# Optimization experiments

Measured on AMD Instinct MI355X. Metric: run time of the kernel, lower is better.

## Reference

```python
import jax, jax.numpy as jnp
import numpy as np

D_MODEL = 1024
NUM_HEADS = 16
DEPTH = D_MODEL // NUM_HEADS
MAX_LEN = 5000


def _make_pe(d_model=D_MODEL, max_len=MAX_LEN):
    # Faithful to torch PositionalEncoding: pe shape [max_len, 1, d_model]
    position = np.arange(max_len, dtype=np.float32)[:, None]
    div_term = np.exp(np.arange(0, d_model, 2, dtype=np.float32) * (-np.log(10000.0) / d_model))
    pe = np.zeros((max_len, d_model), dtype=np.float32)
    pe[:, 0::2] = np.sin(position * div_term)
    pe[:, 1::2] = np.cos(position * div_term)
    return jnp.asarray(pe[:, None, :])  # [max_len, 1, d_model]


def setup_inputs() -> dict:
    key = jax.random.key(0)
    ks = jax.random.split(key, 11)
    B, S, D = 4, 2048, D_MODEL
    s = 1.0 / np.sqrt(D)
    inp = {
        "v": jax.random.normal(ks[0], (B, S, D), jnp.float32),
        "k": jax.random.normal(ks[1], (B, S, D), jnp.float32),
        "q": jax.random.normal(ks[2], (B, S, D), jnp.float32),
        "wq_w": jax.random.normal(ks[3], (D, D), jnp.float32) * s,
        "wq_b": jnp.zeros((D,), jnp.float32),
        "wk_w": jax.random.normal(ks[4], (D, D), jnp.float32) * s,
        "wk_b": jnp.zeros((D,), jnp.float32),
        "wv_w": jax.random.normal(ks[5], (D, D), jnp.float32) * s,
        "wv_b": jnp.zeros((D,), jnp.float32),
        "dense_w": jax.random.normal(ks[6], (D, D), jnp.float32) * s,
        "dense_b": jnp.zeros((D,), jnp.float32),
        "pe": _make_pe(),
    }
    return inp


def _split_heads(x, B):
    # [B, S, D] -> [B, H, S, depth]
    return x.reshape(B, -1, NUM_HEADS, DEPTH).transpose(0, 2, 1, 3)


def reference(v, k, q, wq_w, wq_b, wk_w, wk_b, wv_w, wv_b, dense_w, dense_b, pe):
    B = q.shape[0]
    # Faithful bug-reproduction: pe[:batch] has shape [B, 1, D], broadcast over seq.
    pe_b = pe[:B]  # [B, 1, D]
    q = q + pe_b
    k = k + pe_b
    v = v + pe_b
    # Linear layers (torch: x @ W.T + b)
    qh = _split_heads(q @ wq_w.T + wq_b, B)  # [B,H,Sq,d]
    kh = _split_heads(k @ wk_w.T + wk_b, B)  # [B,H,Sk,d]
    vh = _split_heads(v @ wv_w.T + wv_b, B)  # [B,H,Sk,d]
    scale = 1.0 / jnp.sqrt(jnp.float32(DEPTH))
    logits = jnp.einsum("bhqd,bhkd->bhqk", qh, kh) * scale
    attn = jax.nn.softmax(logits, axis=-1)
    out = jnp.einsum("bhqk,bhkd->bhqd", attn, vh)
    out = out.transpose(0, 2, 1, 3).reshape(B, -1, D_MODEL)
    return out @ dense_w.T + dense_b
```

## Files before the change

### kernel.cpp

```cpp
#include <hip/hip_runtime.h>
#include <hip/hip_bf16.h>

typedef short short8 __attribute__((ext_vector_type(8)));
typedef float f32x4 __attribute__((ext_vector_type(4)));
typedef float f32x16 __attribute__((ext_vector_type(16)));
typedef unsigned int uint4v __attribute__((ext_vector_type(4)));

#define MFMA16(a, b, c) __builtin_amdgcn_mfma_f32_16x16x32_bf16(a, b, c, 0, 0, 0)
#define MFMA32(a, b, c) __builtin_amdgcn_mfma_f32_32x32x16_bf16(a, b, c, 0, 0, 0)

typedef __attribute__((address_space(1))) const unsigned int gas_u32;
typedef __attribute__((address_space(3))) unsigned int las_u32;

__device__ inline void gll16(const void* g, void* l) {
    __builtin_amdgcn_global_load_lds((gas_u32*)g, (las_u32*)l, 16, 0, 0);
}

__device__ inline unsigned short f2bf(float f) {
    unsigned u = __builtin_bit_cast(unsigned, f);
    u += 0x7fff + ((u >> 16) & 1);
    return (unsigned short)(u >> 16);
}

__device__ inline unsigned pk_trunc(float a, float b) {
    unsigned ua = __builtin_bit_cast(unsigned, a);
    unsigned ub = __builtin_bit_cast(unsigned, b);
    return (ua >> 16) | (ub & 0xFFFF0000u);
}

__device__ inline float exp2_fast(float x) {
#if __has_builtin(__builtin_amdgcn_exp2f)
    return __builtin_amdgcn_exp2f(x);
#else
    float r; asm("v_exp_f32 %0, %1" : "=v"(r) : "v"(x)); return r;
#endif
}

__device__ inline void pl32_swap(unsigned &a, unsigned &b) {
    asm volatile("v_permlane32_swap_b32 %0, %1" : "+v"(a), "+v"(b));
}

__global__ void pe_cast3(const float* __restrict__ q, const float* __restrict__ k,
                         const float* __restrict__ v, const float* __restrict__ pe,
                         unsigned short* __restrict__ oq, unsigned short* __restrict__ ok,
                         unsigned short* __restrict__ ov) {
    const float* x = (blockIdx.y == 0) ? q : (blockIdx.y == 1) ? k : v;
    unsigned short* o = (blockIdx.y == 0) ? oq : (blockIdx.y == 1) ? ok : ov;
    int i = blockIdx.x * 256 + threadIdx.x;
    long e = (long)i * 4;
    int b = (int)(e >> 21);
    int d = (int)(e & 1023);
    float4 xv = reinterpret_cast<const float4*>(x)[i];
    float4 pv = *reinterpret_cast<const float4*>(pe + b * 1024 + d);
    ushort4 r;
    r.x = f2bf(xv.x + pv.x); r.y = f2bf(xv.y + pv.y);
    r.z = f2bf(xv.z + pv.z); r.w = f2bf(xv.w + pv.w);
    reinterpret_cast<ushort4*>(o)[i] = r;
}

__global__ void wcast4(const float* __restrict__ w0, const float* __restrict__ w1,
                       const float* __restrict__ w2, const float* __restrict__ w3,
                       unsigned short* __restrict__ o0) {
    const float* w = (blockIdx.y == 0) ? w0 : (blockIdx.y == 1) ? w1
                   : (blockIdx.y == 2) ? w2 : w3;
    unsigned short* o = o0 + (size_t)blockIdx.y * 1024 * 1024;
    int i = blockIdx.x * 256 + threadIdx.x;
    float4 xv = reinterpret_cast<const float4*>(w)[i];
    ushort4 r;
    r.x = f2bf(xv.x); r.y = f2bf(xv.y); r.z = f2bf(xv.z); r.w = f2bf(xv.w);
    reinterpret_cast<ushort4*>(o)[i] = r;
}

__global__ __launch_bounds__(256) void gemm_qkv(const unsigned short* __restrict__ X0,
                                                const unsigned short* __restrict__ W0,
                                                const float* __restrict__ bq,
                                                const float* __restrict__ bk,
                                                const float* __restrict__ bv,
                                                unsigned short* __restrict__ oq,
                                                unsigned short* __restrict__ ok,
                                                unsigned short* __restrict__ ov,
                                                float qscale) {
    const int K = 1024;
    int z = blockIdx.z;
    const unsigned short* A = X0 + (size_t)z * 8192 * 1024;
    const unsigned short* W = W0 + (size_t)z * 1024 * 1024;
    const float* bias = (z == 0) ? bq : (z == 1) ? bk : bv;
    unsigned short* out = (z == 0) ? oq : (z == 1) ? ok : ov;
    float scale = (z == 0) ? qscale : 1.0f;

    __shared__ unsigned short lsA[128 * 32];
    __shared__ unsigned short lsB[128 * 32];
    int tid = threadIdx.x;
    int wave = tid >> 6, lane = tid & 63, lg = lane >> 4, l15 = lane & 15;
    int brow = blockIdx.x * 128;
    int bcol = blockIdx.y * 128;
    int wr = wave >> 1, wc = wave & 1;

    f32x4 zero4 = {0.f, 0.f, 0.f, 0.f};
    f32x4 acc[4][4];
#pragma unroll
    for (int m = 0; m < 4; ++m)
#pragma unroll
        for (int n = 0; n < 4; ++n) acc[m][n] = zero4;

    for (int k0 = 0; k0 < K; k0 += 32) {
#pragma unroll
        for (int j = 0; j < 2; ++j) {
            int c = j * 256 + wave * 64 + lane;
            const unsigned short* srcA = A + ((long)(brow + (c >> 2)) * K + k0 + (c & 3) * 8);
            const unsigned short* srcB = W + ((long)(bcol + (c >> 2)) * K + k0 + (c & 3) * 8);
            char* dstA = (char*)lsA + (j * 256 + wave * 64) * 16;
            char* dstB = (char*)lsB + (j * 256 + wave * 64) * 16;
            gll16(srcA, dstA);
            gll16(srcB, dstB);
        }
        __syncthreads();
        short8 af[4], bf_[4];
#pragma unroll
        for (int m = 0; m < 4; ++m) {
            int row = wr * 64 + m * 16 + l15;
            af[m] = *(const short8*)((const char*)lsA + row * 64 + lg * 16);
        }
#pragma unroll
        for (int n = 0; n < 4; ++n) {
            int col = wc * 64 + n * 16 + l15;
            bf_[n] = *(const short8*)((const char*)lsB + col * 64 + lg * 16);
        }
#pragma unroll
        for (int m = 0; m < 4; ++m)
#pragma unroll
            for (int n = 0; n < 4; ++n) acc[m][n] = MFMA16(af[m], bf_[n], acc[m][n]);
        __syncthreads();
    }

#pragma unroll
    for (int m = 0; m < 4; ++m)
#pragma unroll
        for (int n = 0; n < 4; ++n) {
            int col = bcol + wc * 64 + n * 16 + l15;
            float bv_ = bias[col];
#pragma unroll
            for (int r = 0; r < 4; ++r) {
                int row = brow + wr * 64 + m * 16 + lg * 4 + r;
                float v = (acc[m][n][r] + bv_) * scale;
                int b = row >> 11, s = row & 2047;
                if (z < 2) {
                    int h = col >> 6, d = col & 63;
                    out[(((long)(b * 16 + h) * 2048 + s) * 64 + d)] = f2bf(v);
                } else {
                    out[((long)(b * 1024 + col)) * 2048 + s] = f2bf(v);
                }
            }
        }
}

__global__ __launch_bounds__(256) void gemm_dense(const unsigned short* __restrict__ A,
                                                  const unsigned short* __restrict__ W,
                                                  const float* __restrict__ bias,
                                                  float* __restrict__ out) {
    const int K = 1024;
    __shared__ unsigned short lsA[128 * 32];
    __shared__ unsigned short lsB[128 * 32];
    int tid = threadIdx.x;
    int wave = tid >> 6, lane = tid & 63, lg = lane >> 4, l15 = lane & 15;
    int brow = blockIdx.x * 128;
    int bcol = blockIdx.y * 128;
    int wr = wave >> 1, wc = wave & 1;

    f32x4 zero4 = {0.f, 0.f, 0.f, 0.f};
    f32x4 acc[4][4];
#pragma unroll
    for (int m = 0; m < 4; ++m)
#pragma unroll
        for (int n = 0; n < 4; ++n) acc[m][n] = zero4;

    for (int k0 = 0; k0 < K; k0 += 32) {
#pragma unroll
        for (int j = 0; j < 2; ++j) {
            int c = j * 256 + wave * 64 + lane;
            const unsigned short* srcA = A + ((long)(brow + (c >> 2)) * K + k0 + (c & 3) * 8);
            const unsigned short* srcB = W + ((long)(bcol + (c >> 2)) * K + k0 + (c & 3) * 8);
            char* dstA = (char*)lsA + (j * 256 + wave * 64) * 16;
            char* dstB = (char*)lsB + (j * 256 + wave * 64) * 16;
            gll16(srcA, dstA);
            gll16(srcB, dstB);
        }
        __syncthreads();
        short8 af[4], bf_[4];
#pragma unroll
        for (int m = 0; m < 4; ++m) {
            int row = wr * 64 + m * 16 + l15;
            af[m] = *(const short8*)((const char*)lsA + row * 64 + lg * 16);
        }
#pragma unroll
        for (int n = 0; n < 4; ++n) {
            int col = wc * 64 + n * 16 + l15;
            bf_[n] = *(const short8*)((const char*)lsB + col * 64 + lg * 16);
        }
#pragma unroll
        for (int m = 0; m < 4; ++m)
#pragma unroll
            for (int n = 0; n < 4; ++n) acc[m][n] = MFMA16(af[m], bf_[n], acc[m][n]);
        __syncthreads();
    }

#pragma unroll
    for (int m = 0; m < 4; ++m)
#pragma unroll
        for (int n = 0; n < 4; ++n) {
            int col = bcol + wc * 64 + n * 16 + l15;
            float bv = bias[col];
#pragma unroll
            for (int r = 0; r < 4; ++r) {
                int row = brow + wr * 64 + m * 16 + lg * 4 + r;
                out[(long)row * 1024 + col] = acc[m][n][r] + bv;
            }
        }
}

__global__ __launch_bounds__(256, 2) void attn_kernel(const unsigned short* __restrict__ Qh,
                                                      const unsigned short* __restrict__ Kh,
                                                      const unsigned short* __restrict__ Vt,
                                                      unsigned short* __restrict__ Om) {
    const int S = 2048;
    const int NT = S / 64;
    int flat = blockIdx.x;
    int nf_ = (flat & 7) * 64 + (flat >> 3);
    int qt = nf_ & 7;
    int bh = nf_ >> 3;
    int b = bh >> 4, h = bh & 15;

    int tid = threadIdx.x, wave = tid >> 6, lane = tid & 63;
    int l31 = lane & 31, hi = lane >> 5;

    __shared__ __align__(16) unsigned short Kl[3][4096];
    __shared__ __align__(16) unsigned short Vtl[3][4096];

    const unsigned short* Qb = Qh + (long)bh * S * 64;
    const unsigned short* Kb = Kh + (long)bh * S * 64;
    const unsigned short* Vb = Vt + (long)bh * 64 * S;

    int colS = ((((tid & 7) * 16) ^ (((tid >> 3) & 7) << 4)) >> 1);
    const unsigned short* srcK = Kb + (tid >> 3) * 64 + colS;
    const unsigned short* srcV = Vb + (tid >> 3) * 2048 + colS;

    short8 aq[2][4];
    {
        const unsigned short* qrow = Qb + (long)(qt * 256 + wave * 64 + l31) * 64 + hi * 8;
#pragma unroll
        for (int qf = 0; qf < 2; ++qf)
#pragma unroll
            for (int s = 0; s < 4; ++s)
                aq[qf][s] = *(const short8*)(qrow + qf * 32 * 64 + s * 16);
    }

    f32x16 oacc[2][2], lacc[2];
#pragma unroll
    for (int r = 0; r < 16; ++r) {
        oacc[0][0][r] = 0.f; oacc[0][1][r] = 0.f;
        oacc[1][0][r] = 0.f; oacc[1][1][r] = 0.f;
        lacc[0][r] = 0.f; lacc[1][r] = 0.f;
    }

    const short8 ones8 = {0x3F80, 0x3F80, 0x3F80, 0x3F80, 0x3F80, 0x3F80, 0x3F80, 0x3F80};

    int rb0 = l31 * 128;
    int swz = (l31 & 7) << 4;

#define STAGE(kt, bi) do {                                              \
        const unsigned short* sk = srcK + (kt) * 4096;                  \
        gll16(sk,         (char*)Kl[bi] + wave * 1024);                 \
        gll16(sk + 2048,  (char*)Kl[bi] + 4096 + wave * 1024);          \
        const unsigned short* sv = srcV + (kt) * 64;                    \
        gll16(sv,         (char*)Vtl[bi] + wave * 1024);                \
        gll16(sv + 65536, (char*)Vtl[bi] + 4096 + wave * 1024);         \
    } while (0)

    STAGE(0, 0);
    STAGE(1, 1);

    int bi = 0, sb = 2;
    for (int kt = 0; kt < NT; ++kt) {
        if (kt == NT - 1) { asm volatile("s_waitcnt vmcnt(0)" ::: "memory"); }
        else              { asm volatile("s_waitcnt vmcnt(4)" ::: "memory"); }
        __builtin_amdgcn_s_barrier();
        if (kt < NT - 2) STAGE(kt + 2, sb);

        const char* KlC = (const char*)Kl[bi];
        const char* VlC = (const char*)Vtl[bi];

        f32x16 sacc[2][2];
#pragma unroll
        for (int r = 0; r < 16; ++r) {
            sacc[0][0][r] = 0.f; sacc[0][1][r] = 0.f;
            sacc[1][0][r] = 0.f; sacc[1][1][r] = 0.f;
        }
#pragma unroll
        for (int blk = 0; blk < 2; ++blk)
#pragma unroll
            for (int s = 0; s < 4; ++s) {
                short8 kf = *(const short8*)(KlC + blk * 4096 + rb0 + ((32 * s + 16 * hi) ^ swz));
                sacc[0][blk] = MFMA32(kf, aq[0][s], sacc[0][blk]);
                sacc[1][blk] = MFMA32(kf, aq[1][s], sacc[1][blk]);
            }

#pragma unroll
        for (int qf = 0; qf < 2; ++qf)
#pragma unroll
            for (int blk = 0; blk < 2; ++blk)
#pragma unroll
                for (int r = 0; r < 16; ++r) sacc[qf][blk][r] = exp2_fast(sacc[qf][blk][r]);

#pragma unroll
        for (int s = 0; s < 4; ++s) {
            const int blk = s >> 1, base = (s & 1) * 8;
            short8 pa[2];
#pragma unroll
            for (int qf = 0; qf < 2; ++qf) {
                unsigned q0 = pk_trunc(sacc[qf][blk][base + 0], sacc[qf][blk][base + 1]);
                unsigned q1 = pk_trunc(sacc[qf][blk][base + 2], sacc[qf][blk][base + 3]);
                unsigned q2 = pk_trunc(sacc[qf][blk][base + 4], sacc[qf][blk][base + 5]);
                unsigned q3 = pk_trunc(sacc[qf][blk][base + 6], sacc[qf][blk][base + 7]);
                pl32_swap(q0, q2);
                pl32_swap(q1, q3);
                uint4v pw; pw[0] = q0; pw[1] = q1; pw[2] = q2; pw[3] = q3;
                pa[qf] = __builtin_bit_cast(short8, pw);
            }
#pragma unroll
            for (int dblk = 0; dblk < 2; ++dblk) {
                short8 vf = *(const short8*)(VlC + dblk * 4096 + rb0 + ((32 * s + 16 * hi) ^ swz));
                oacc[0][dblk] = MFMA32(pa[0], vf, oacc[0][dblk]);
                oacc[1][dblk] = MFMA32(pa[1], vf, oacc[1][dblk]);
            }
            lacc[0] = MFMA32(pa[0], ones8, lacc[0]);
            lacc[1] = MFMA32(pa[1], ones8, lacc[1]);
        }
        bi = (bi == 2) ? 0 : bi + 1;
        sb = (sb == 2) ? 0 : sb + 1;
    }
#undef STAGE

#pragma unroll
    for (int qf = 0; qf < 2; ++qf) {
        float inv[16];
#pragma unroll
        for (int r = 0; r < 16; ++r) inv[r] = 1.0f / lacc[qf][r];
        int qrow0 = qt * 256 + wave * 64 + qf * 32 + 4 * hi;
#pragma unroll
        for (int dblk = 0; dblk < 2; ++dblk)
#pragma unroll
            for (int r = 0; r < 16; ++r) {
                int qrow = qrow0 + (r & 3) + 8 * (r >> 2);
                int d = h * 64 + dblk * 32 + l31;
                float v = oacc[qf][dblk][r] * inv[r];
                Om[((long)b * 2048 + qrow) * 1024 + d] = f2bf(v);
            }
    }
}

extern "C" void kernel_launch(void* const* d_in, const int* in_sizes, int n_in,
                              void* d_out, int out_size, void* d_ws, size_t ws_size,
                              hipStream_t stream) {
    const float* v_in = (const float*)d_in[0];
    const float* k_in = (const float*)d_in[1];
    const float* q_in = (const float*)d_in[2];
    const float* wq_w = (const float*)d_in[3];
    const float* wq_b = (const float*)d_in[4];
    const float* wk_w = (const float*)d_in[5];
    const float* wk_b = (const float*)d_in[6];
    const float* wv_w = (const float*)d_in[7];
    const float* wv_b = (const float*)d_in[8];
    const float* wd_w = (const float*)d_in[9];
    const float* wd_b = (const float*)d_in[10];
    const float* pe   = (const float*)d_in[11];

    const long SZ = 8192L * 1024 * 2;
    char* ws = (char*)d_ws;
    unsigned short* xq = (unsigned short*)(ws + 0);
    unsigned short* xk = (unsigned short*)(ws + SZ);
    unsigned short* xv = (unsigned short*)(ws + 2 * SZ);
    unsigned short* qh = (unsigned short*)(ws + 3 * SZ);
    unsigned short* kh = (unsigned short*)(ws + 4 * SZ);
    unsigned short* vt = (unsigned short*)(ws + 5 * SZ);
    unsigned short* wqb16 = (unsigned short*)(ws + 6 * SZ);

    pe_cast3<<<dim3(8192, 3), 256, 0, stream>>>(q_in, k_in, v_in, pe, xq, xk, xv);
    wcast4<<<dim3(1024, 4), 256, 0, stream>>>(wq_w, wk_w, wv_w, wd_w, wqb16);

    const float QSCALE = 0.125f * 1.44269504088896f;
    gemm_qkv<<<dim3(64, 8, 3), 256, 0, stream>>>(xq, wqb16, wq_b, wk_b, wv_b,
                                                 qh, kh, vt, QSCALE);
    unsigned short* om = xq;
    attn_kernel<<<512, 256, 0, stream>>>(qh, kh, vt, om);
    gemm_dense<<<dim3(64, 8), 256, 0, stream>>>(om, wqb16 + 3L * 1024 * 1024, wd_b,
                                                (float*)d_out);
}
```

Before: 219.6 us.

## Replace QKV and dense GEMMs with double-buffered 32x32 MFMA templated kernel

Replaces the two 128x128 GEMM kernels with one templated kernel that uses 512 threads, 256-wide N tiles (BM 256 for QKV, 128 for dense) and BK=64. Global-to-LDS loads are double-buffered with a single sync per k-step, and the LDS layout is XOR-swizzled to avoid bank conflicts. It also moves from 16x16x32 to 32x32x16 MFMA. The intent is more data reuse per tile, fewer barriers and better overlap of loads with compute. The cost is much more LDS (about 128KB for the QKV variant), which may limit occupancy, and fewer blocks for the dense GEMM.

```diff
diff --git a/kernel.cpp b/kernel.cpp
--- a/kernel.cpp
+++ b/kernel.cpp
@@ -2,11 +2,9 @@
 #include <hip/hip_bf16.h>
 
 typedef short short8 __attribute__((ext_vector_type(8)));
-typedef float f32x4 __attribute__((ext_vector_type(4)));
 typedef float f32x16 __attribute__((ext_vector_type(16)));
 typedef unsigned int uint4v __attribute__((ext_vector_type(4)));
 
-#define MFMA16(a, b, c) __builtin_amdgcn_mfma_f32_16x16x32_bf16(a, b, c, 0, 0, 0)
 #define MFMA32(a, b, c) __builtin_amdgcn_mfma_f32_32x32x16_bf16(a, b, c, 0, 0, 0)
 
 typedef __attribute__((address_space(1))) const unsigned int gas_u32;
@@ -71,149 +69,109 @@
     reinterpret_cast<ushort4*>(o)[i] = r;
 }
 
-__global__ __launch_bounds__(256) void gemm_qkv(const unsigned short* __restrict__ X0,
+template <int BM, int MF, int MODE>
+__global__ __launch_bounds__(512, 2) void gemm2(const unsigned short* __restrict__ A0,
                                                 const unsigned short* __restrict__ W0,
                                                 const float* __restrict__ bq,
                                                 const float* __restrict__ bk,
                                                 const float* __restrict__ bv,
-                                                unsigned short* __restrict__ oq,
-                                                unsigned short* __restrict__ ok,
-                                                unsigned short* __restrict__ ov,
+                                                void* __restrict__ oq,
+                                                void* __restrict__ ok,
+                                                void* __restrict__ ov,
                                                 float qscale) {
-    const int K = 1024;
-    int z = blockIdx.z;
-    const unsigned short* A = X0 + (size_t)z * 8192 * 1024;
+    const int NT = 16;
+    constexpr int AR = BM / 64;
+    __shared__ __align__(16) unsigned short lsA[2][BM * 64];
+    __shared__ __align__(16) unsigned short lsB[2][256 * 64];
+
+    int z = (MODE == 3) ? blockIdx.z : 0;
+    const unsigned short* A = A0 + (size_t)z * 8192 * 1024;
     const unsigned short* W = W0 + (size_t)z * 1024 * 1024;
-    const float* bias = (z == 0) ? bq : (z == 1) ? bk : bv;
-    unsigned short* out = (z == 0) ? oq : (z == 1) ? ok : ov;
-    float scale = (z == 0) ? qscale : 1.0f;
-
-    __shared__ unsigned short lsA[128 * 32];
-    __shared__ unsigned short lsB[128 * 32];
-    int tid = threadIdx.x;
-    int wave = tid >> 6, lane = tid & 63, lg = lane >> 4, l15 = lane & 15;
-    int brow = blockIdx.x * 128;
-    int bcol = blockIdx.y * 128;
-    int wr = wave >> 1, wc = wave & 1;
-
-    f32x4 zero4 = {0.f, 0.f, 0.f, 0.f};
-    f32x4 acc[4][4];
-#pragma unroll
-    for (int m = 0; m < 4; ++m)
-#pragma unroll
-        for (int n = 0; n < 4; ++n) acc[m][n] = zero4;
-
-    for (int k0 = 0; k0 < K; k0 += 32) {
-#pragma unroll
-        for (int j = 0; j < 2; ++j) {
-            int c = j * 256 + wave * 64 + lane;
-            const unsigned short* srcA = A + ((long)(brow + (c >> 2)) * K + k0 + (c & 3) * 8);
-            const unsigned short* srcB = W + ((long)(bcol + (c >> 2)) * K + k0 + (c & 3) * 8);
-            char* dstA = (char*)lsA + (j * 256 + wave * 64) * 16;
-            char* dstB = (char*)lsB + (j * 256 + wave * 64) * 16;
-            gll16(srcA, dstA);
-            gll16(srcB, dstB);
+    const float* bias = (MODE == 3) ? ((z == 0) ? bq : (z == 1) ? bk : bv) : bq;
+    float scale = (MODE == 3 && z == 0) ? qscale : 1.0f;
+
+    int tid = threadIdx.x, wave = tid >> 6, lane = tid & 63;
+    int l31 = lane & 31, hi = lane >> 5;
+    int wr = wave >> 2, wc = wave & 3;
+    int brow = blockIdx.x * BM;
+    int bcol = blockIdx.y * 256;
+
+    int rowt = tid >> 3;
+    int colsw = (tid & 7) * 8 ^ ((rowt & 7) << 3);
+    const unsigned short* srcA = A + (long)(brow + rowt) * 1024 + colsw;
+    const unsigned short* srcB = W + (long)(bcol + rowt) * 1024 + colsw;
+
+    f32x16 acc[MF][2];
+#pragma unroll
+    for (int mf = 0; mf < MF; ++mf)
+#pragma unroll
+        for (int nf = 0; nf < 2; ++nf)
+#pragma unroll
+            for (int r = 0; r < 16; ++r) acc[mf][nf][r] = 0.f;
+
+#define STG(t, bi) do {                                                       \
+        _Pragma("unroll")                                                     \
+        for (int rr = 0; rr < AR; ++rr)                                       \
+            gll16(srcA + (t) * 64 + rr * 65536,                               \
+                  (char*)lsA[bi] + (rr * 512 + wave * 64) * 16);              \
+        _Pragma("unroll")                                                     \
+        for (int rr = 0; rr < 4; ++rr)                                        \
+            gll16(srcB + (t) * 64 + rr * 65536,                               \
+                  (char*)lsB[bi] + (rr * 512 + wave * 64) * 16);              \
+    } while (0)
+
+    STG(0, 0);
+    __syncthreads();
+
+    int cur = 0;
+    for (int t = 0; t < NT; ++t) {
+        if (t < NT - 1) STG(t + 1, cur ^ 1);
+
+        const char* KA = (const char*)lsA[cur];
+        const char* KB = (const char*)lsB[cur];
+#pragma unroll
+        for (int ks = 0; ks < 4; ++ks) {
+            int cofs = (ks * 32 + hi * 16) ^ ((l31 & 7) << 4);
+            short8 af[MF], bf[2];
+#pragma unroll
+            for (int mf = 0; mf < MF; ++mf)
+                af[mf] = *(const short8*)(KA + (wr * (MF * 32) + mf * 32 + l31) * 128 + cofs);
+#pragma unroll
+            for (int nf = 0; nf < 2; ++nf)
+                bf[nf] = *(const short8*)(KB + (wc * 64 + nf * 32 + l31) * 128 + cofs);
+#pragma unroll
+            for (int mf = 0; mf < MF; ++mf)
+#pragma unroll
+                for (int nf = 0; nf < 2; ++nf)
+                    acc[mf][nf] = MFMA32(af[mf], bf[nf], acc[mf][nf]);
         }
         __syncthreads();
-        short8 af[4], bf_[4];
-#pragma unroll
-        for (int m = 0; m < 4; ++m) {
-            int row = wr * 64 + m * 16 + l15;
-            af[m] = *(const short8*)((const char*)lsA + row * 64 + lg * 16);
-        }
-#pragma unroll
-        for (int n = 0; n < 4; ++n) {
-            int col = wc * 64 + n * 16 + l15;
-            bf_[n] = *(const short8*)((const char*)lsB + col * 64 + lg * 16);
-        }
-#pragma unroll
-        for (int m = 0; m < 4; ++m)
-#pragma unroll
-            for (int n = 0; n < 4; ++n) acc[m][n] = MFMA16(af[m], bf_[n], acc[m][n]);
-        __syncthreads();
-    }
-
-#pragma unroll
-    for (int m = 0; m < 4; ++m)
-#pragma unroll
-        for (int n = 0; n < 4; ++n) {
-            int col = bcol + wc * 64 + n * 16 + l15;
+        cur ^= 1;
+    }
+#undef STG
+
+    void* out = (MODE == 3) ? ((z == 0) ? oq : (z == 1) ? ok : ov) : oq;
+#pragma unroll
+    for (int mf = 0; mf < MF; ++mf)
+#pragma unroll
+        for (int nf = 0; nf < 2; ++nf) {
+            int col = bcol + wc * 64 + nf * 32 + l31;
             float bv_ = bias[col];
 #pragma unroll
-            for (int r = 0; r < 4; ++r) {
-                int row = brow + wr * 64 + m * 16 + lg * 4 + r;
-                float v = (acc[m][n][r] + bv_) * scale;
-                int b = row >> 11, s = row & 2047;
-                if (z < 2) {
-                    int h = col >> 6, d = col & 63;
-                    out[(((long)(b * 16 + h) * 2048 + s) * 64 + d)] = f2bf(v);
+            for (int r = 0; r < 16; ++r) {
+                int row = brow + wr * (MF * 32) + mf * 32 + (r & 3) + 8 * (r >> 2) + 4 * hi;
+                float v = (acc[mf][nf][r] + bv_) * scale;
+                if (MODE == 1) {
+                    ((float*)out)[(long)row * 1024 + col] = v;
                 } else {
-                    out[((long)(b * 1024 + col)) * 2048 + s] = f2bf(v);
+                    int b = row >> 11, s = row & 2047;
+                    if (z < 2) {
+                        int h = col >> 6, d = col & 63;
+                        ((unsigned short*)out)[(((long)(b * 16 + h) * 2048 + s) * 64 + d)] = f2bf(v);
+                    } else {
+                        ((unsigned short*)out)[((long)(b * 1024 + col)) * 2048 + s] = f2bf(v);
+                    }
                 }
-            }
-        }
-}
-
-__global__ __launch_bounds__(256) void gemm_dense(const unsigned short* __restrict__ A,
-                                                  const unsigned short* __restrict__ W,
-                                                  const float* __restrict__ bias,
-                                                  float* __restrict__ out) {
-    const int K = 1024;
-    __shared__ unsigned short lsA[128 * 32];
-    __shared__ unsigned short lsB[128 * 32];
-    int tid = threadIdx.x;
-    int wave = tid >> 6, lane = tid & 63, lg = lane >> 4, l15 = lane & 15;
-    int brow = blockIdx.x * 128;
-    int bcol = blockIdx.y * 128;
-    int wr = wave >> 1, wc = wave & 1;
-
-    f32x4 zero4 = {0.f, 0.f, 0.f, 0.f};
-    f32x4 acc[4][4];
-#pragma unroll
-    for (int m = 0; m < 4; ++m)
-#pragma unroll
-        for (int n = 0; n < 4; ++n) acc[m][n] = zero4;
-
-    for (int k0 = 0; k0 < K; k0 += 32) {
-#pragma unroll
-        for (int j = 0; j < 2; ++j) {
-            int c = j * 256 + wave * 64 + lane;
-            const unsigned short* srcA = A + ((long)(brow + (c >> 2)) * K + k0 + (c & 3) * 8);
-            const unsigned short* srcB = W + ((long)(bcol + (c >> 2)) * K + k0 + (c & 3) * 8);
-            char* dstA = (char*)lsA + (j * 256 + wave * 64) * 16;
-            char* dstB = (char*)lsB + (j * 256 + wave * 64) * 16;
-            gll16(srcA, dstA);
-            gll16(srcB, dstB);
-        }
-        __syncthreads();
-        short8 af[4], bf_[4];
-#pragma unroll
-        for (int m = 0; m < 4; ++m) {
-            int row = wr * 64 + m * 16 + l15;
-            af[m] = *(const short8*)((const char*)lsA + row * 64 + lg * 16);
-        }
-#pragma unroll
-        for (int n = 0; n < 4; ++n) {
-            int col = wc * 64 + n * 16 + l15;
-            bf_[n] = *(const short8*)((const char*)lsB + col * 64 + lg * 16);
-        }
-#pragma unroll
-        for (int m = 0; m < 4; ++m)
-#pragma unroll
-            for (int n = 0; n < 4; ++n) acc[m][n] = MFMA16(af[m], bf_[n], acc[m][n]);
-        __syncthreads();
-    }
-
-#pragma unroll
-    for (int m = 0; m < 4; ++m)
-#pragma unroll
-        for (int n = 0; n < 4; ++n) {
-            int col = bcol + wc * 64 + n * 16 + l15;
-            float bv = bias[col];
-#pragma unroll
-            for (int r = 0; r < 4; ++r) {
-                int row = brow + wr * 64 + m * 16 + lg * 4 + r;
-                out[(long)row * 1024 + col] = acc[m][n][r] + bv;
             }
         }
 }
@@ -388,10 +346,12 @@
     wcast4<<<dim3(1024, 4), 256, 0, stream>>>(wq_w, wk_w, wv_w, wd_w, wqb16);
 
     const float QSCALE = 0.125f * 1.44269504088896f;
-    gemm_qkv<<<dim3(64, 8, 3), 256, 0, stream>>>(xq, wqb16, wq_b, wk_b, wv_b,
-                                                 qh, kh, vt, QSCALE);
+    gemm2<256, 4, 3><<<dim3(32, 4, 3), 512, 0, stream>>>(
+        xq, wqb16, wq_b, wk_b, wv_b, qh, kh, vt, QSCALE);
+
     unsigned short* om = xq;
     attn_kernel<<<512, 256, 0, stream>>>(qh, kh, vt, om);
-    gemm_dense<<<dim3(64, 8), 256, 0, stream>>>(om, wqb16 + 3L * 1024 * 1024, wd_b,
-                                                (float*)d_out);
-}
+
+    gemm2<128, 2, 1><<<dim3(64, 4, 1), 512, 0, stream>>>(
+        om, wqb16 + 3L * 1024 * 1024, wd_b, nullptr, nullptr, d_out, nullptr, nullptr, 1.0f);
+}
```

New measurement: 231.3 us. 5.3% more time.
